# Kernel tuning notes

Hardware: AMD Instinct MI355X
Metric: run time of the kernel (lower is better)

## Reference

```python
import jax, jax.numpy as jnp
import numpy as np

HEAD_DIM = 128
INFTY_APPROX = 1e+30
ROTARY_BASE = 10000.0

B, T, M = 2, 2048, 1024
H = M // HEAD_DIM  # 8


def setup_inputs() -> dict:
    key = jax.random.key(0)
    ks = jax.random.split(key, 5)
    x = jax.random.normal(ks[0], (B, T, M), dtype=jnp.float32)
    # mu-param inits: wq zeros in the original; use small random here for a
    # non-degenerate numerical baseline, scaled like kv_init = d_model**-0.5
    scale = M ** (-0.5)
    wq = jax.random.normal(ks[1], (M, H, HEAD_DIM), dtype=jnp.float32) * scale
    wk = jax.random.normal(ks[2], (M, H, HEAD_DIM), dtype=jnp.float32) * scale
    wv = jax.random.normal(ks[3], (M, H, HEAD_DIM), dtype=jnp.float32) * scale
    wo = jax.random.normal(ks[4], (H, HEAD_DIM, M), dtype=jnp.float32) * scale
    return {"x": x, "wq": wq, "wk": wk, "wv": wv, "wo": wo}


def _rotary(x, base=ROTARY_BASE):
    # x: [..., T, W]; non-interpretable RoPE over even/odd halves of W
    length, width = x.shape[-2], x.shape[-1]
    half = width // 2
    positions = jnp.arange(length)[:, None].astype(x.dtype)          # [T,1]
    ang_freqs = jnp.power(base, -jnp.arange(half) / half)[None, :]   # [1,half]
    radians = positions * ang_freqs                                  # [T,half]
    cos = jnp.cos(radians).astype(x.dtype)
    sin = jnp.sin(radians).astype(x.dtype)
    even, odd = jnp.split(x, 2, axis=-1)
    return jnp.concatenate([even * cos - odd * sin,
                            even * sin + odd * cos], axis=-1)


def _fractional_rotary(x):
    # rotary on first half of head dim, passthrough on the rest
    rot, skip = jnp.split(x, 2, axis=-1)
    return jnp.concatenate([_rotary(rot), skip], axis=-1)


def reference(x, wq, wk, wv, wo):
    q = jnp.einsum('bim,mhd->bhid', x, wq)
    k = jnp.einsum('bim,mhd->bhid', x, wk)
    v = jnp.einsum('bim,mhd->bhid', x, wv)
    q = _fractional_rotary(q)
    k = _fractional_rotary(k)
    # mu-param attention: scale by 1/HEAD_DIM (not 1/sqrt(D))
    s = jnp.einsum('bhid,bhjd->bhij', q, k) / HEAD_DIM
    i = jnp.arange(T)[:, None]
    j = jnp.arange(T)[None, :]
    mask = (i < j).astype(s.dtype)  # strictly-upper-triangular
    s = s - jnp.asarray(INFTY_APPROX, dtype=s.dtype) * mask
    p = jax.nn.softmax(s, axis=-1)
    o = jnp.einsum('bhij,bhjd->bhid', p, v)
    r = jnp.einsum('bhid,hdm->bim', o, wo)
    return r
```

## Files before the change

### kernel.cpp

```cpp
#include <hip/hip_runtime.h>

#define T_SEQ 2048
#define MDL   1024
#define NH    8
#define HD    128
#define SPLIT 6

typedef __bf16 bf16;
typedef __bf16 bf16x8 __attribute__((ext_vector_type(8)));
typedef __bf16 bf16x4 __attribute__((ext_vector_type(4)));
typedef float  f32x4  __attribute__((ext_vector_type(4)));

#define GLB(p) ((const __attribute__((address_space(1))) void*)(p))
#define LDS(p) ((__attribute__((address_space(3))) void*)(p))

#if __has_builtin(__builtin_amdgcn_exp2f)
#define EXP2(x) __builtin_amdgcn_exp2f(x)
#else
#define EXP2(x) __expf((x) * 0.6931471805599453f)
#endif

#define QSCALE 0.011271055f


__global__ __launch_bounds__(256) void convert_x_kernel(
    const float* __restrict__ x, bf16* __restrict__ xb)
{
    size_t i = ((size_t)blockIdx.x * 256 + threadIdx.x) * 8;
    float4 v0 = *(const float4*)(x + i);
    float4 v1 = *(const float4*)(x + i + 4);
    bf16x8 o;
    o[0]=(bf16)v0.x; o[1]=(bf16)v0.y; o[2]=(bf16)v0.z; o[3]=(bf16)v0.w;
    o[4]=(bf16)v1.x; o[5]=(bf16)v1.y; o[6]=(bf16)v1.z; o[7]=(bf16)v1.w;
    *(bf16x8*)(xb + i) = o;
}

__global__ __launch_bounds__(256) void transpose_w_kernel(
    const float* __restrict__ wq, const float* __restrict__ wk,
    const float* __restrict__ wv, const float* __restrict__ wo,
    bf16* __restrict__ Wt, bf16* __restrict__ Wot)
{
    __shared__ bf16 t_lds[64 * 72];
    const int bx = blockIdx.x;
    const int sec = bx >> 8;
    const int tile = bx & 255;
    const int k0 = (tile >> 4) * 64, n0 = (tile & 15) * 64;
    const float* src = sec == 0 ? wq : sec == 1 ? wk : sec == 2 ? wv : wo;
    bf16* dst = sec < 3 ? (Wt + (size_t)sec * MDL * MDL) : Wot;

    const int tid = threadIdx.x;
    const int ir = tid >> 2, jc = (tid & 3) * 16;
    const float* sp = src + (size_t)(k0 + ir) * MDL + n0 + jc;
    #pragma unroll
    for (int c = 0; c < 4; ++c) {
        float4 v = *(const float4*)(sp + c * 4);
        bf16x4 o; o[0]=(bf16)v.x; o[1]=(bf16)v.y; o[2]=(bf16)v.z; o[3]=(bf16)v.w;
        *(bf16x4*)&t_lds[ir * 72 + jc + c * 4] = o;
    }
    __syncthreads();
    bf16x8 o0, o1;
    #pragma unroll
    for (int jj = 0; jj < 8; ++jj) {
        o0[jj] = t_lds[(jc + jj) * 72 + ir];
        o1[jj] = t_lds[(jc + 8 + jj) * 72 + ir];
    }
    bf16* dp = dst + (size_t)(n0 + ir) * MDL + k0 + jc;
    *(bf16x8*)dp = o0;
    *(bf16x8*)(dp + 8) = o1;
}

__global__ __launch_bounds__(256) void qkv_rope_kernel(
    const bf16* __restrict__ xb, const bf16* __restrict__ Wt,
    bf16* __restrict__ Qb, bf16* __restrict__ Kt, bf16* __restrict__ Vt)
{
    __shared__ bf16 smem[8192];
    bf16* a_lds = smem;
    bf16* b_lds = smem + 4096;

    const int tid = threadIdx.x, bx = blockIdx.x;
    const int nt = bx % 24, mt = bx / 24;
    const int n0 = nt * 128, m0 = mt * 128;
    const int section = n0 >> 10;
    const int h = (n0 & 1023) >> 7;

    const int lane = tid & 63, w = tid >> 6;
    const int quad = lane >> 4, l15 = lane & 15;
    const int wr = w >> 1, wc = w & 1;
    const int lrow = lane >> 2, lsub = lane & 3;

    const bf16* gA = xb + (size_t)m0 * MDL + lsub * 8;
    const bf16* gB = Wt + (size_t)n0 * MDL + lsub * 8;

    f32x4 acc[4][4] = {};

    for (int k0 = 0; k0 < MDL; k0 += 32) {
        #pragma unroll
        for (int i = 0; i < 2; ++i) {
            const int ch = w * 2 + i;
            const int row = ch * 16 + lrow;
            __builtin_amdgcn_global_load_lds(GLB(gA + (size_t)row * MDL + k0),
                                             LDS(&a_lds[ch * 16 * 32]), 16, 0, 0);
            __builtin_amdgcn_global_load_lds(GLB(gB + (size_t)row * MDL + k0),
                                             LDS(&b_lds[ch * 16 * 32]), 16, 0, 0);
        }
        __syncthreads();

        bf16x8 af[4], bfr[4];
        #pragma unroll
        for (int mi = 0; mi < 4; ++mi)
            af[mi] = *(const bf16x8*)&a_lds[(wr * 64 + mi * 16 + l15) * 32 + quad * 8];
        #pragma unroll
        for (int ni = 0; ni < 4; ++ni)
            bfr[ni] = *(const bf16x8*)&b_lds[(wc * 64 + ni * 16 + l15) * 32 + quad * 8];
        #pragma unroll
        for (int mi = 0; mi < 4; ++mi)
            #pragma unroll
            for (int ni = 0; ni < 4; ++ni)
                acc[mi][ni] = __builtin_amdgcn_mfma_f32_16x16x32_bf16(af[mi], bfr[ni], acc[mi][ni], 0, 0, 0);
        __syncthreads();
    }

    const int bdx = m0 >> 11;
    const int t0 = m0 & (T_SEQ - 1);
    const int bh = bdx * NH + h;

    if (section == 2) {
        #pragma unroll
        for (int c = 0; c < 2; ++c) {
            if (wc == c) {
                #pragma unroll
                for (int mi = 0; mi < 4; ++mi)
                    #pragma unroll
                    for (int r = 0; r < 4; ++r) {
                        int p = 16 * quad + 4 * r + mi;
                        int base = (wr * 8 + (p >> 3)) * 512 + (p & 7);
                        #pragma unroll
                        for (int ni = 0; ni < 4; ++ni)
                            smem[base + (ni * 16 + l15) * 8] = (bf16)acc[mi][ni][r];
                    }
            }
            __syncthreads();
            {
                const int t8 = tid >> 4;
                bf16* vp = Vt + ((size_t)(bh * 32 + (t0 >> 6) + (t8 >> 3))) * 8192
                              + (t8 & 7) * 1024 + c * 512 + (tid & 15) * 32;
                #pragma unroll
                for (int k = 0; k < 4; ++k)
                    *(bf16x8*)(vp + k * 8) = *(const bf16x8*)&smem[tid * 32 + k * 8];
            }
            __syncthreads();
        }
        return;
    }

    float fr_n[2];
    #pragma unroll
    for (int ni = 0; ni < 2; ++ni)
        fr_n[ni] = __expf(-(float)(ni * 16 + l15) * 0.28782313662425573f);

    if (section == 0) {
        #pragma unroll
        for (int mi = 0; mi < 4; ++mi) {
            #pragma unroll
            for (int r = 0; r < 4; ++r) {
                int t = t0 + wr * 64 + mi * 16 + quad * 4 + r;
                bf16* orow = Qb + ((size_t)bh * T_SEQ + t) * HD;
                if (wc == 0) {
                    #pragma unroll
                    for (int ni = 0; ni < 2; ++ni) {
                        int d = ni * 16 + l15;
                        float ang = (float)t * fr_n[ni];
                        float sn = __sinf(ang), cs = __cosf(ang);
                        float ev = acc[mi][ni][r];
                        float ov = acc[mi][ni + 2][r];
                        orow[d]      = (bf16)((ev * cs - ov * sn) * QSCALE);
                        orow[d + 32] = (bf16)((ev * sn + ov * cs) * QSCALE);
                    }
                } else {
                    #pragma unroll
                    for (int ni = 0; ni < 4; ++ni)
                        orow[64 + ni * 16 + l15] = (bf16)(acc[mi][ni][r] * QSCALE);
                }
            }
        }
    } else {
        #pragma unroll
        for (int c = 0; c < 2; ++c) {
            if (wr == c) {
                #pragma unroll
                for (int mi = 0; mi < 4; ++mi) {
                    #pragma unroll
                    for (int r = 0; r < 4; ++r) {
                        int tl = mi * 16 + quad * 4 + r;
                        int t = t0 + c * 64 + tl;
                        if (wc == 0) {
                            #pragma unroll
                            for (int ni = 0; ni < 2; ++ni) {
                                int d = ni * 16 + l15;
                                float ang = (float)t * fr_n[ni];
                                float sn = __sinf(ang), cs = __cosf(ang);
                                float ev = acc[mi][ni][r];
                                float ov = acc[mi][ni + 2][r];
                                smem[(d >> 3) * 512 + tl * 8 + (d & 7)] = (bf16)(ev * cs - ov * sn);
                                int d2 = d + 32;
                                smem[(d2 >> 3) * 512 + tl * 8 + (d2 & 7)] = (bf16)(ev * sn + ov * cs);
                            }
                        } else {
                            #pragma unroll
                            for (int ni = 0; ni < 4; ++ni) {
                                int d = 64 + ni * 16 + l15;
                                smem[(d >> 3) * 512 + tl * 8 + (d & 7)] = (bf16)acc[mi][ni][r];
                            }
                        }
                    }
                }
            }
            __syncthreads();
            {
                bf16* kp = Kt + ((size_t)(bh * 32 + (t0 >> 6) + c)) * 8192 + tid * 32;
                #pragma unroll
                for (int k = 0; k < 4; ++k)
                    *(bf16x8*)(kp + k * 8) = *(const bf16x8*)&smem[tid * 32 + k * 8];
            }
            __syncthreads();
        }
    }
}

__global__ __launch_bounds__(256) void attn_kernel(
    const bf16* __restrict__ Qb, const bf16* __restrict__ Kt,
    const bf16* __restrict__ Vt, bf16* __restrict__ PO, float* __restrict__ Pl)
{
    __shared__ bf16 k_lds[8192];
    __shared__ bf16 v_lds[8192];
    __shared__ bf16 p_lds[4][32 * 72];

    const int tid = threadIdx.x, lane = tid & 63, w = tid >> 6;
    const int quad = lane >> 4, l15 = lane & 15;
    const int bx = blockIdx.x;
    const int s0 = bx % SPLIT;
    const int ip = (bx / SPLIT) & 7;
    const int bh = bx / (SPLIT * 8);
    const int tA = 2 * ip + 2;

    const bf16* Kbh = Kt + (size_t)bh * 32 * 8192;
    const bf16* Vbh = Vt + (size_t)bh * 32 * 8192;

    bf16x8 qf[2][4];
    f32x4 Of[2][8];
    float l_r[2][4];

    int g = s0;

    #pragma unroll 1
    for (int phase = 0; phase < 2; ++phase) {
        const int qt = (phase == 0) ? ip : 15 - ip;
        const int gend = (phase == 0) ? tA : 34;
        const int gbase = (phase == 0) ? 0 : tA;
        if (g >= gend) continue;

        #pragma unroll
        for (int mi = 0; mi < 2; ++mi) {
            const bf16* qrow = Qb + ((size_t)bh * T_SEQ + qt * 128 + w * 32 + mi * 16 + l15) * HD + quad * 8;
            #pragma unroll
            for (int kk = 0; kk < 4; ++kk)
                qf[mi][kk] = *(const bf16x8*)(qrow + kk * 32);
            #pragma unroll
            for (int di = 0; di < 8; ++di) Of[mi][di] = (f32x4){0.f, 0.f, 0.f, 0.f};
            #pragma unroll
            for (int r = 0; r < 4; ++r) l_r[mi][r] = 0.f;
        }

        #pragma unroll 1
        for (; g < gend; g += SPLIT) {
            const int jt = g - gbase;
            __syncthreads();
            const bf16* ktile = Kbh + jt * 8192;
            const bf16* vtile = Vbh + jt * 8192;
            #pragma unroll
            for (int ii = 0; ii < 4; ++ii) {
                const int j = w * 4 + ii;
                __builtin_amdgcn_global_load_lds(GLB(ktile + j * 512 + lane * 8),
                                                 LDS(&k_lds[j * 512]), 16, 0, 0);
                __builtin_amdgcn_global_load_lds(GLB(vtile + j * 512 + lane * 8),
                                                 LDS(&v_lds[j * 512]), 16, 0, 0);
            }
            __syncthreads();

            f32x4 sa[2][4] = {};
            #pragma unroll
            for (int kk = 0; kk < 4; ++kk) {
                bf16x8 kb[4];
                #pragma unroll
                for (int ni = 0; ni < 4; ++ni)
                    kb[ni] = *(const bf16x8*)&k_lds[(kk * 4 + quad) * 512 + (ni * 16 + l15) * 8];
                #pragma unroll
                for (int ni = 0; ni < 4; ++ni)
                    #pragma unroll
                    for (int mi = 0; mi < 2; ++mi)
                        sa[mi][ni] = __builtin_amdgcn_mfma_f32_16x16x32_bf16(qf[mi][kk], kb[ni], sa[mi][ni], 0, 0, 0);
            }

            const bool diag = (jt >= 2 * qt);
            #pragma unroll
            for (int mi = 0; mi < 2; ++mi) {
                const int rowb = w * 32 + mi * 16 + quad * 4;
                #pragma unroll
                for (int r = 0; r < 4; ++r) {
                    float ps = 0.f;
                    bf16x4 pq;
                    #pragma unroll
                    for (int ni = 0; ni < 4; ++ni) {
                        float pv = EXP2(sa[mi][ni][r]);
                        if (diag && (jt * 64 + ni * 16 + l15) > (qt * 128 + rowb + r)) pv = 0.f;
                        ps += pv;
                        pq[ni] = (bf16)pv;
                    }
                    *(bf16x4*)&p_lds[w][(mi * 16 + quad * 4 + r) * 72 + l15 * 4] = pq;
                    l_r[mi][r] += ps;
                }
            }

            #pragma unroll
            for (int kk = 0; kk < 2; ++kk) {
                bf16x8 pa[2];
                #pragma unroll
                for (int mi = 0; mi < 2; ++mi)
                    pa[mi] = *(const bf16x8*)&p_lds[w][(mi * 16 + l15) * 72 + kk * 32 + quad * 8];
                #pragma unroll
                for (int di = 0; di < 8; ++di) {
                    bf16x8 vb = *(const bf16x8*)&v_lds[(kk * 4 + quad) * 1024 + (di * 16 + l15) * 8];
                    #pragma unroll
                    for (int mi = 0; mi < 2; ++mi)
                        Of[mi][di] = __builtin_amdgcn_mfma_f32_16x16x32_bf16(pa[mi], vb, Of[mi][di], 0, 0, 0);
                }
            }
        }

        const size_t slot = ((size_t)bh * 16 + qt) * SPLIT + s0;
        #pragma unroll
        for (int mi = 0; mi < 2; ++mi) {
            #pragma unroll
            for (int r = 0; r < 4; ++r) {
                float ls = l_r[mi][r];
                ls += __shfl_xor(ls, 1); ls += __shfl_xor(ls, 2);
                ls += __shfl_xor(ls, 4); ls += __shfl_xor(ls, 8);
                const int row = w * 32 + mi * 16 + quad * 4 + r;
                if (l15 == 0) Pl[slot * 128 + row] = ls;
                bf16* pr = PO + (slot * 128 + row) * 128;
                #pragma unroll
                for (int di = 0; di < 8; ++di)
                    pr[di * 16 + l15] = (bf16)Of[mi][di][r];
            }
        }
    }
}

__global__ __launch_bounds__(256) void attn_combine_kernel(
    const bf16* __restrict__ PO, const float* __restrict__ Pl,
    bf16* __restrict__ Ob)
{
    const int idx = blockIdx.x * 256 + threadIdx.x;
    const int dcol = (idx & 15) * 8;
    const int rowg = idx >> 4;
    const int bh = rowg >> 11, qrow = rowg & 2047;
    const int qt = qrow >> 7, row = qrow & 127;
    const int ns = (qt == 0) ? 2 : ((qt == 1) ? 4 : SPLIT);

    float acc[8] = {};
    float l = 0.f;
    for (int s = 0; s < ns; ++s) {
        const size_t base = (((size_t)bh * 16 + qt) * SPLIT + s) * 128 + row;
        bf16x8 po = *(const bf16x8*)&PO[base * 128 + dcol];
        #pragma unroll
        for (int jj = 0; jj < 8; ++jj) acc[jj] += (float)po[jj];
        l += Pl[base];
    }
    const float inv = 1.f / l;
    const int b = bh >> 3, hh = bh & 7, t = qt * 128 + row;
    bf16x8 o;
    #pragma unroll
    for (int jj = 0; jj < 8; ++jj) o[jj] = (bf16)(acc[jj] * inv);
    *(bf16x8*)(Ob + ((size_t)(b * T_SEQ + t) * NH + hh) * HD + dcol) = o;
}

__global__ __launch_bounds__(256) void out_proj_kernel(
    const bf16* __restrict__ Ob, const bf16* __restrict__ Wot,
    float* __restrict__ out)
{
    __shared__ bf16 a_lds[128 * 32];
    __shared__ bf16 b_lds[128 * 32];

    const int tid = threadIdx.x, bx = blockIdx.x;
    const int nt = bx & 7, mt = bx >> 3;
    const int n0 = nt * 128, m0 = mt * 128;

    const int lane = tid & 63, w = tid >> 6;
    const int quad = lane >> 4, l15 = lane & 15;
    const int wr = w >> 1, wc = w & 1;
    const int lrow = lane >> 2, lsub = lane & 3;

    const bf16* gA = Ob  + (size_t)m0 * MDL + lsub * 8;
    const bf16* gB = Wot + (size_t)n0 * MDL + lsub * 8;

    f32x4 acc[4][4] = {};

    for (int k0 = 0; k0 < MDL; k0 += 32) {
        #pragma unroll
        for (int i = 0; i < 2; ++i) {
            const int ch = w * 2 + i;
            const int row = ch * 16 + lrow;
            __builtin_amdgcn_global_load_lds(GLB(gA + (size_t)row * MDL + k0),
                                             LDS(&a_lds[ch * 16 * 32]), 16, 0, 0);
            __builtin_amdgcn_global_load_lds(GLB(gB + (size_t)row * MDL + k0),
                                             LDS(&b_lds[ch * 16 * 32]), 16, 0, 0);
        }
        __syncthreads();

        bf16x8 af[4], bfr[4];
        #pragma unroll
        for (int mi = 0; mi < 4; ++mi)
            af[mi] = *(const bf16x8*)&a_lds[(wr * 64 + mi * 16 + l15) * 32 + quad * 8];
        #pragma unroll
        for (int ni = 0; ni < 4; ++ni)
            bfr[ni] = *(const bf16x8*)&b_lds[(wc * 64 + ni * 16 + l15) * 32 + quad * 8];
        #pragma unroll
        for (int mi = 0; mi < 4; ++mi)
            #pragma unroll
            for (int ni = 0; ni < 4; ++ni)
                acc[mi][ni] = __builtin_amdgcn_mfma_f32_16x16x32_bf16(af[mi], bfr[ni], acc[mi][ni], 0, 0, 0);
        __syncthreads();
    }

    #pragma unroll
    for (int mi = 0; mi < 4; ++mi)
        #pragma unroll
        for (int r = 0; r < 4; ++r) {
            int row_g = m0 + wr * 64 + mi * 16 + quad * 4 + r;
            float* crow = out + (size_t)row_g * MDL + n0;
            #pragma unroll
            for (int ni = 0; ni < 4; ++ni)
                crow[wc * 64 + ni * 16 + l15] = acc[mi][ni][r];
        }
}

extern "C" void kernel_launch(void* const* d_in, const int* in_sizes, int n_in,
                              void* d_out, int out_size, void* d_ws, size_t ws_size,
                              hipStream_t stream) {
    const float* x  = (const float*)d_in[0];
    const float* wq = (const float*)d_in[1];
    const float* wk = (const float*)d_in[2];
    const float* wv = (const float*)d_in[3];
    const float* wo = (const float*)d_in[4];
    float* out = (float*)d_out;

    const size_t NTOK = (size_t)2 * NH * T_SEQ * HD;
    bf16*  Qb  = (bf16*)d_ws;
    bf16*  Kt  = Qb + NTOK;
    bf16*  Vt  = Kt + NTOK;
    bf16*  Ob  = Vt + NTOK;
    bf16*  Wot = Ob + NTOK;
    bf16*  PO  = Wot + (size_t)MDL * MDL;
    float* Pl  = (float*)(PO + (size_t)16 * 16 * SPLIT * 128 * 128);

    bf16* xbuf = (bf16*)d_out;
    bf16* Wt   = xbuf + (size_t)4096 * MDL;

    transpose_w_kernel<<<1024, 256, 0, stream>>>(wq, wk, wv, wo, Wt, Wot);
    convert_x_kernel<<<2048, 256, 0, stream>>>(x, xbuf);
    qkv_rope_kernel<<<768, 256, 0, stream>>>(xbuf, Wt, Qb, Kt, Vt);
    attn_kernel<<<16 * 8 * SPLIT, 256, 0, stream>>>(Qb, Kt, Vt, PO, Pl);
    attn_combine_kernel<<<2048, 256, 0, stream>>>(PO, Pl, Ob);
    out_proj_kernel<<<256, 256, 0, stream>>>(Ob, Wot, out);
}
```

Measured before the change: 207.9 us.

## Prefetch K/V tiles through registers, reduce split count, fuse prep kernels

The attention kernel now loads the next K/V tile into registers while computing on the current tile, then stores it to LDS. This replaces the synchronous global-to-LDS loads and hides memory latency. The two phases are flattened into one loop. The split count drops from 6 to 4, which gives fewer partial outputs to combine but less parallelism. The x conversion and the weight transpose are merged into a single launch to save launch overhead. The register prefetch raises register pressure.

```diff
diff --git a/kernel.cpp b/kernel.cpp
--- a/kernel.cpp
+++ b/kernel.cpp
@@ -4,7 +4,7 @@
 #define MDL   1024
 #define NH    8
 #define HD    128
-#define SPLIT 6
+#define SPLIT 4
 
 typedef __bf16 bf16;
 typedef __bf16 bf16x8 __attribute__((ext_vector_type(8)));
@@ -23,32 +23,31 @@
 #define QSCALE 0.011271055f
 
 
-__global__ __launch_bounds__(256) void convert_x_kernel(
-    const float* __restrict__ x, bf16* __restrict__ xb)
-{
-    size_t i = ((size_t)blockIdx.x * 256 + threadIdx.x) * 8;
-    float4 v0 = *(const float4*)(x + i);
-    float4 v1 = *(const float4*)(x + i + 4);
-    bf16x8 o;
-    o[0]=(bf16)v0.x; o[1]=(bf16)v0.y; o[2]=(bf16)v0.z; o[3]=(bf16)v0.w;
-    o[4]=(bf16)v1.x; o[5]=(bf16)v1.y; o[6]=(bf16)v1.z; o[7]=(bf16)v1.w;
-    *(bf16x8*)(xb + i) = o;
-}
-
-__global__ __launch_bounds__(256) void transpose_w_kernel(
+__global__ __launch_bounds__(256) void prep_kernel(
+    const float* __restrict__ x,
     const float* __restrict__ wq, const float* __restrict__ wk,
     const float* __restrict__ wv, const float* __restrict__ wo,
-    bf16* __restrict__ Wt, bf16* __restrict__ Wot)
+    bf16* __restrict__ xb, bf16* __restrict__ Wt, bf16* __restrict__ Wot)
 {
     __shared__ bf16 t_lds[64 * 72];
-    const int bx = blockIdx.x;
+    const int tid = threadIdx.x;
+    if (blockIdx.x < 2048) {
+        size_t i = ((size_t)blockIdx.x * 256 + tid) * 8;
+        float4 v0 = *(const float4*)(x + i);
+        float4 v1 = *(const float4*)(x + i + 4);
+        bf16x8 o;
+        o[0]=(bf16)v0.x; o[1]=(bf16)v0.y; o[2]=(bf16)v0.z; o[3]=(bf16)v0.w;
+        o[4]=(bf16)v1.x; o[5]=(bf16)v1.y; o[6]=(bf16)v1.z; o[7]=(bf16)v1.w;
+        *(bf16x8*)(xb + i) = o;
+        return;
+    }
+    const int bx = blockIdx.x - 2048;
     const int sec = bx >> 8;
     const int tile = bx & 255;
     const int k0 = (tile >> 4) * 64, n0 = (tile & 15) * 64;
     const float* src = sec == 0 ? wq : sec == 1 ? wk : sec == 2 ? wv : wo;
     bf16* dst = sec < 3 ? (Wt + (size_t)sec * MDL * MDL) : Wot;
 
-    const int tid = threadIdx.x;
     const int ir = tid >> 2, jc = (tid & 3) * 16;
     const float* sp = src + (size_t)(k0 + ir) * MDL + n0 + jc;
     #pragma unroll
@@ -246,100 +245,126 @@
     const bf16* Kbh = Kt + (size_t)bh * 32 * 8192;
     const bf16* Vbh = Vt + (size_t)bh * 32 * 8192;
 
+    bf16x8 kreg[4], vreg[4];
     bf16x8 qf[2][4];
     f32x4 Of[2][8];
     float l_r[2][4];
 
-    int g = s0;
+    auto fetch = [&](int g) {
+        const int jt = (g < tA) ? g : g - tA;
+        const bf16* kt = Kbh + (size_t)jt * 8192 + tid * 8;
+        const bf16* vt = Vbh + (size_t)jt * 8192 + tid * 8;
+        #pragma unroll
+        for (int k = 0; k < 4; ++k) {
+            kreg[k] = *(const bf16x8*)(kt + k * 2048);
+            vreg[k] = *(const bf16x8*)(vt + k * 2048);
+        }
+    };
+
+    fetch(s0);
+    int pqt = -1;
 
     #pragma unroll 1
-    for (int phase = 0; phase < 2; ++phase) {
-        const int qt = (phase == 0) ? ip : 15 - ip;
-        const int gend = (phase == 0) ? tA : 34;
-        const int gbase = (phase == 0) ? 0 : tA;
-        if (g >= gend) continue;
-
+    for (int g = s0; g < 34; g += SPLIT) {
+        const int ph = (g >= tA);
+        const int qt = ph ? 15 - ip : ip;
+        const int jt = ph ? g - tA : g;
+
+        if (qt != pqt) {
+            if (pqt >= 0) {
+                const size_t slot = ((size_t)bh * 16 + pqt) * SPLIT + s0;
+                #pragma unroll
+                for (int mi = 0; mi < 2; ++mi)
+                    #pragma unroll
+                    for (int r = 0; r < 4; ++r) {
+                        float ls = l_r[mi][r];
+                        ls += __shfl_xor(ls, 1); ls += __shfl_xor(ls, 2);
+                        ls += __shfl_xor(ls, 4); ls += __shfl_xor(ls, 8);
+                        const int row = w * 32 + mi * 16 + quad * 4 + r;
+                        if (l15 == 0) Pl[slot * 128 + row] = ls;
+                        bf16* pr = PO + (slot * 128 + row) * 128;
+                        #pragma unroll
+                        for (int di = 0; di < 8; ++di)
+                            pr[di * 16 + l15] = (bf16)Of[mi][di][r];
+                    }
+            }
+            #pragma unroll
+            for (int mi = 0; mi < 2; ++mi) {
+                const bf16* qrow = Qb + ((size_t)bh * T_SEQ + qt * 128 + w * 32 + mi * 16 + l15) * HD + quad * 8;
+                #pragma unroll
+                for (int kk = 0; kk < 4; ++kk)
+                    qf[mi][kk] = *(const bf16x8*)(qrow + kk * 32);
+                #pragma unroll
+                for (int di = 0; di < 8; ++di) Of[mi][di] = (f32x4){0.f, 0.f, 0.f, 0.f};
+                #pragma unroll
+                for (int r = 0; r < 4; ++r) l_r[mi][r] = 0.f;
+            }
+            pqt = qt;
+        }
+
+        __syncthreads();
+        #pragma unroll
+        for (int k = 0; k < 4; ++k) {
+            *(bf16x8*)&k_lds[k * 2048 + tid * 8] = kreg[k];
+            *(bf16x8*)&v_lds[k * 2048 + tid * 8] = vreg[k];
+        }
+        if (g + SPLIT < 34) fetch(g + SPLIT);
+        __syncthreads();
+
+        f32x4 sa[2][4] = {};
+        #pragma unroll
+        for (int kk = 0; kk < 4; ++kk) {
+            bf16x8 kb[4];
+            #pragma unroll
+            for (int ni = 0; ni < 4; ++ni)
+                kb[ni] = *(const bf16x8*)&k_lds[(kk * 4 + quad) * 512 + (ni * 16 + l15) * 8];
+            #pragma unroll
+            for (int ni = 0; ni < 4; ++ni)
+                #pragma unroll
+                for (int mi = 0; mi < 2; ++mi)
+                    sa[mi][ni] = __builtin_amdgcn_mfma_f32_16x16x32_bf16(qf[mi][kk], kb[ni], sa[mi][ni], 0, 0, 0);
+        }
+
+        const bool diag = (jt >= 2 * qt);
         #pragma unroll
         for (int mi = 0; mi < 2; ++mi) {
-            const bf16* qrow = Qb + ((size_t)bh * T_SEQ + qt * 128 + w * 32 + mi * 16 + l15) * HD + quad * 8;
-            #pragma unroll
-            for (int kk = 0; kk < 4; ++kk)
-                qf[mi][kk] = *(const bf16x8*)(qrow + kk * 32);
-            #pragma unroll
-            for (int di = 0; di < 8; ++di) Of[mi][di] = (f32x4){0.f, 0.f, 0.f, 0.f};
-            #pragma unroll
-            for (int r = 0; r < 4; ++r) l_r[mi][r] = 0.f;
-        }
-
-        #pragma unroll 1
-        for (; g < gend; g += SPLIT) {
-            const int jt = g - gbase;
-            __syncthreads();
-            const bf16* ktile = Kbh + jt * 8192;
-            const bf16* vtile = Vbh + jt * 8192;
-            #pragma unroll
-            for (int ii = 0; ii < 4; ++ii) {
-                const int j = w * 4 + ii;
-                __builtin_amdgcn_global_load_lds(GLB(ktile + j * 512 + lane * 8),
-                                                 LDS(&k_lds[j * 512]), 16, 0, 0);
-                __builtin_amdgcn_global_load_lds(GLB(vtile + j * 512 + lane * 8),
-                                                 LDS(&v_lds[j * 512]), 16, 0, 0);
-            }
-            __syncthreads();
-
-            f32x4 sa[2][4] = {};
-            #pragma unroll
-            for (int kk = 0; kk < 4; ++kk) {
-                bf16x8 kb[4];
-                #pragma unroll
-                for (int ni = 0; ni < 4; ++ni)
-                    kb[ni] = *(const bf16x8*)&k_lds[(kk * 4 + quad) * 512 + (ni * 16 + l15) * 8];
-                #pragma unroll
-                for (int ni = 0; ni < 4; ++ni)
-                    #pragma unroll
-                    for (int mi = 0; mi < 2; ++mi)
-                        sa[mi][ni] = __builtin_amdgcn_mfma_f32_16x16x32_bf16(qf[mi][kk], kb[ni], sa[mi][ni], 0, 0, 0);
-            }
-
-            const bool diag = (jt >= 2 * qt);
-            #pragma unroll
-            for (int mi = 0; mi < 2; ++mi) {
-                const int rowb = w * 32 + mi * 16 + quad * 4;
-                #pragma unroll
-                for (int r = 0; r < 4; ++r) {
-                    float ps = 0.f;
-                    bf16x4 pq;
-                    #pragma unroll
-                    for (int ni = 0; ni < 4; ++ni) {
-                        float pv = EXP2(sa[mi][ni][r]);
-                        if (diag && (jt * 64 + ni * 16 + l15) > (qt * 128 + rowb + r)) pv = 0.f;
-                        ps += pv;
-                        pq[ni] = (bf16)pv;
-                    }
-                    *(bf16x4*)&p_lds[w][(mi * 16 + quad * 4 + r) * 72 + l15 * 4] = pq;
-                    l_r[mi][r] += ps;
+            const int rowb = w * 32 + mi * 16 + quad * 4;
+            #pragma unroll
+            for (int r = 0; r < 4; ++r) {
+                float ps = 0.f;
+                bf16x4 pq;
+                #pragma unroll
+                for (int ni = 0; ni < 4; ++ni) {
+                    float pv = EXP2(sa[mi][ni][r]);
+                    if (diag && (jt * 64 + ni * 16 + l15) > (qt * 128 + rowb + r)) pv = 0.f;
+                    ps += pv;
+                    pq[ni] = (bf16)pv;
                 }
-            }
-
-            #pragma unroll
-            for (int kk = 0; kk < 2; ++kk) {
-                bf16x8 pa[2];
+                *(bf16x4*)&p_lds[w][(mi * 16 + quad * 4 + r) * 72 + l15 * 4] = pq;
+                l_r[mi][r] += ps;
+            }
+        }
+
+        #pragma unroll
+        for (int kk = 0; kk < 2; ++kk) {
+            bf16x8 pa[2];
+            #pragma unroll
+            for (int mi = 0; mi < 2; ++mi)
+                pa[mi] = *(const bf16x8*)&p_lds[w][(mi * 16 + l15) * 72 + kk * 32 + quad * 8];
+            #pragma unroll
+            for (int di = 0; di < 8; ++di) {
+                bf16x8 vb = *(const bf16x8*)&v_lds[(kk * 4 + quad) * 1024 + (di * 16 + l15) * 8];
                 #pragma unroll
                 for (int mi = 0; mi < 2; ++mi)
-                    pa[mi] = *(const bf16x8*)&p_lds[w][(mi * 16 + l15) * 72 + kk * 32 + quad * 8];
-                #pragma unroll
-                for (int di = 0; di < 8; ++di) {
-                    bf16x8 vb = *(const bf16x8*)&v_lds[(kk * 4 + quad) * 1024 + (di * 16 + l15) * 8];
-                    #pragma unroll
-                    for (int mi = 0; mi < 2; ++mi)
-                        Of[mi][di] = __builtin_amdgcn_mfma_f32_16x16x32_bf16(pa[mi], vb, Of[mi][di], 0, 0, 0);
-                }
-            }
-        }
-
-        const size_t slot = ((size_t)bh * 16 + qt) * SPLIT + s0;
-        #pragma unroll
-        for (int mi = 0; mi < 2; ++mi) {
+                    Of[mi][di] = __builtin_amdgcn_mfma_f32_16x16x32_bf16(pa[mi], vb, Of[mi][di], 0, 0, 0);
+            }
+        }
+    }
+
+    {
+        const size_t slot = ((size_t)bh * 16 + pqt) * SPLIT + s0;
+        #pragma unroll
+        for (int mi = 0; mi < 2; ++mi)
             #pragma unroll
             for (int r = 0; r < 4; ++r) {
                 float ls = l_r[mi][r];
@@ -352,7 +377,6 @@
                 for (int di = 0; di < 8; ++di)
                     pr[di * 16 + l15] = (bf16)Of[mi][di][r];
             }
-        }
     }
 }
 
@@ -466,8 +490,7 @@
     bf16* xbuf = (bf16*)d_out;
     bf16* Wt   = xbuf + (size_t)4096 * MDL;
 
-    transpose_w_kernel<<<1024, 256, 0, stream>>>(wq, wk, wv, wo, Wt, Wot);
-    convert_x_kernel<<<2048, 256, 0, stream>>>(x, xbuf);
+    prep_kernel<<<3072, 256, 0, stream>>>(x, wq, wk, wv, wo, xbuf, Wt, Wot);
     qkv_rope_kernel<<<768, 256, 0, stream>>>(xbuf, Wt, Qb, Kt, Vt);
     attn_kernel<<<16 * 8 * SPLIT, 256, 0, stream>>>(Qb, Kt, Vt, PO, Pl);
     attn_combine_kernel<<<2048, 256, 0, stream>>>(PO, Pl, Ob);
```

Measured after the change: 195.3 us. -6.1%, faster.
